# Performance work log

Measured on AMD Instinct MI355X. Metric: run time of the kernel, lower is better.

## Reference

```python
import jax, jax.numpy as jnp
import numpy as np

N, M = 65536, 512
CTRL = 128
IN_DIM = 128
READ_LEN = M + 6          # [M,1,1,3,1]
WRITE_LEN = 3 * M + 6     # [M,1,1,3,1,M,M]
EPS = 1e-16


def setup_inputs() -> dict:
    key = jax.random.key(0)
    ks = jax.random.split(key, 12)
    s = 0.02
    return {
        "x":   jax.random.normal(ks[0], (4, IN_DIM), jnp.float32),
        "mem": jax.random.normal(ks[1], (N, M), jnp.float32) * 0.05,
        "Wc":  jax.random.normal(ks[2], (CTRL, IN_DIM), jnp.float32) * s,
        "bc":  jnp.zeros((CTRL,), jnp.float32),
        "Wr":  jax.random.normal(ks[3], (READ_LEN, CTRL), jnp.float32) * s,
        "br":  jnp.zeros((READ_LEN,), jnp.float32),
        "Ww":  jax.random.normal(ks[4], (WRITE_LEN, CTRL), jnp.float32) * s,
        "bw":  jnp.zeros((WRITE_LEN,), jnp.float32),
        "W1":  jax.random.normal(ks[5], (200, M + CTRL), jnp.float32) * s,
        "b1":  jnp.zeros((200,), jnp.float32),
        "W2":  jax.random.normal(ks[6], (10, 200), jnp.float32) * s,
        "b2":  jnp.zeros((10,), jnp.float32),
    }


def _address(mem, k, beta, g, s, gamma, w_prev):
    # content + gate + circular shift + sharpen (standard NTM addressing)
    beta = jax.nn.softplus(beta)
    g = jax.nn.sigmoid(g)
    s = jax.nn.softmax(s)                      # (3,)
    gamma = 1.0 + jax.nn.softplus(gamma)
    # cosine similarity against all N memory rows
    dot = mem @ k                              # (N,)
    norms = jnp.sqrt(jnp.sum(mem * mem, axis=1)) * jnp.sqrt(jnp.sum(k * k)) + EPS
    wc = jax.nn.softmax(beta * dot / norms)    # content weights (N,)
    wg = g * wc + (1.0 - g) * w_prev           # gated
    # circular convolution with 3-tap shift kernel s = [s(-1), s(0), s(+1)]
    ws = s[0] * jnp.roll(wg, 1) + s[1] * wg + s[2] * jnp.roll(wg, -1)
    w = ws ** gamma                            # sharpen
    return w / (jnp.sum(w) + EPS)


def _forward(x, mem, Wc, bc, Wr, br, Ww, bw, W1, b1, W2, b2):
    cont = x @ Wc.T + bc                       # controller: (4, 128)
    w0 = jnp.full((N,), 1.0 / N, x.dtype)      # softmax of constant -> uniform

    def step(carry, c_t):
        mem, w_r, w_w = carry
        # ---- write head ----
        ow = c_t @ Ww.T + bw                   # (3M+6,)
        k, b, g, s, y = ow[:M], ow[M], ow[M+1], ow[M+2:M+5], ow[M+5]
        e, a = ow[M+6:2*M+6], ow[2*M+6:]
        w_w = _address(mem, k, b, g, s, y, w_w)
        e = jax.nn.sigmoid(e)
        mem = mem * (1.0 - jnp.outer(w_w, e)) + jnp.outer(w_w, a)
        # ---- read head ----
        orr = c_t @ Wr.T + br                  # (M+6,)
        k, b, g, s, y = orr[:M], orr[M], orr[M+1], orr[M+2:M+5], orr[M+5]
        w_r = _address(mem, k, b, g, s, y, w_r)
        r = w_r @ mem                          # (M,)
        # ---- output MLP ----
        h = jax.nn.relu(jnp.concatenate([c_t, r]) @ W1.T + b1)
        out = h @ W2.T + b2                    # (10,)
        return (mem, w_r, w_w), out

    _, outs = jax.lax.scan(step, (mem, w0, w0), cont)
    return outs                                # (4, 10)


def reference(x, mem, Wc, bc, Wr, br, Ww, bw, W1, b1, W2, b2):
    return _forward(x, mem, Wc, bc, Wr, br, Ww, bw, W1, b1, W2, b2)
```

## Files before the change

kernel.cpp:

```cpp
#include <hip/hip_runtime.h>
#include <math.h>

#define NN    65536
#define CTRLD 128
#define WLEN  1542
#define RLEN  518
#define EPSF  1e-16f
#define UB    2048
#define RPB   32
#define RPW   8

__device__ __forceinline__ float softplusf_(float x){
    return x > 0.f ? x + log1pf(expf(-x)) : log1pf(expf(x));
}
__device__ __forceinline__ float sigmoidf_(float x){ return 1.f/(1.f+expf(-x)); }

__device__ __forceinline__ float blockReduce256(float v, float* red){
    int t = threadIdx.x;
    red[t] = v; __syncthreads();
    for(int s = 128; s; s >>= 1){ if(t < s) red[t] += red[t+s]; __syncthreads(); }
    float r = red[0]; __syncthreads();
    return r;
}
__device__ __forceinline__ void waveReduce3(float& a, float& b, float& c){
    for(int o = 32; o; o >>= 1){
        a += __shfl_down(a,o); b += __shfl_down(b,o); c += __shfl_down(c,o);
    }
}
__device__ __forceinline__ void waveReduce1(float& a){
    for(int o = 32; o; o >>= 1) a += __shfl_down(a,o);
}

__global__ void k_owor(const float* __restrict__ x, const float* __restrict__ Wc,
                       const float* __restrict__ bc,
                       const float* __restrict__ Ww, const float* __restrict__ bw,
                       const float* __restrict__ Wr, const float* __restrict__ br,
                       float* __restrict__ cont,
                       float* __restrict__ kW, float* __restrict__ sW,
                       float* __restrict__ eW, float* __restrict__ aW,
                       float* __restrict__ kR, float* __restrict__ sR){
    __shared__ float cs[512];
    int tid = threadIdx.x;
    for(int q = tid; q < 512; q += 256){
        int t = q >> 7, c = q & 127;
        float acc = bc[c];
        const float* xr = x + t*CTRLD;
        const float* wr = Wc + c*CTRLD;
        for(int d = 0; d < CTRLD; ++d) acc += xr[d]*wr[d];
        cs[q] = acc;
        if(blockIdx.x == 0) cont[q] = acc;
    }
    __syncthreads();
    int idx = blockIdx.x*256 + tid;
    if(idx < 4*WLEN){
        int t = idx / WLEN, o = idx % WLEN;
        float acc = bw[o];
        const float* cr = cs + t*CTRLD;
        const float* wr = Ww + o*CTRLD;
        for(int d = 0; d < CTRLD; ++d) acc += cr[d]*wr[d];
        if(o < 512)       kW[t*512 + o] = acc;
        else if(o < 518)  sW[t*8 + (o-512)] = acc;
        else if(o < 1030) eW[t*512 + (o-518)] = sigmoidf_(acc);
        else              aW[t*512 + (o-1030)] = acc;
    } else {
        int j = idx - 4*WLEN;
        if(j < 4*RLEN){
            int t = j / RLEN, o = j % RLEN;
            float acc = br[o];
            const float* cr = cs + t*CTRLD;
            const float* wr = Wr + o*CTRLD;
            for(int d = 0; d < CTRLD; ++d) acc += cr[d]*wr[d];
            if(o < 512) kR[t*512 + o] = acc;
            else        sR[t*8 + (o-512)] = acc;
        }
    }
}

__global__ void k_prep(const float* __restrict__ kW, const float* __restrict__ kR,
                       float* __restrict__ kn){
    int t = threadIdx.x;
    int wave = t >> 6, lane = t & 63;
    int step = wave >> 1, which = wave & 1;
    const float* base = which ? (kR + step*512) : (kW + step*512);
    float s = 0.f;
    for(int h = 0; h < 8; ++h){ float v = base[lane + h*64]; s += v*v; }
    waveReduce1(s);
    if(lane == 0) kn[wave] = sqrtf(s);
}

template<int CH, bool RP, bool UPD, bool DOTR, bool DOTW>
__global__ __launch_bounds__(256) void k_mega(
    const float* __restrict__ mem0,
    const float* __restrict__ wunWall, const float* __restrict__ pSWall,
    const float* __restrict__ wunRall,
    const float* __restrict__ eW, const float* __restrict__ aW,
    const float* __restrict__ kRc, const float* __restrict__ sRc,
    const float* __restrict__ kWn, const float* __restrict__ sWn,
    const float* __restrict__ kn, int knRidx, int knWidx,
    float* __restrict__ dotRo, float* __restrict__ dotWo, float* __restrict__ n2o,
    float* __restrict__ pZr, float* __restrict__ pZw, float* __restrict__ rp)
{
    constexpr int NW = CH + (UPD ? 1 : 0);
    constexpr int NA = NW > 0 ? NW : 1;
    __shared__ float red[256];
    __shared__ float zsh[4][2];
    __shared__ float rps[4][512];
    int t = threadIdx.x;
    float wnorm[NA];
    #pragma unroll
    for(int j = 0; j < NW; ++j)
        wnorm[j] = 1.f/(blockReduce256(pSWall[j*256 + t], red) + EPSF);

    int wave = t >> 6, lane = t & 63;
    int c0 = lane, c1 = lane + 64;
    float4 ev0[NA], ev1[NA], av0[NA], av1[NA];
    #pragma unroll
    for(int j = 0; j < NW; ++j){
        ev0[j] = ((const float4*)(eW + j*512))[c0];
        ev1[j] = ((const float4*)(eW + j*512))[c1];
        av0[j] = ((const float4*)(aW + j*512))[c0];
        av1[j] = ((const float4*)(aW + j*512))[c1];
    }
    float4 kra, krb, kwa, kwb;
    float betaR = 0.f, betaW = 0.f, knRv = 1.f, knWv = 1.f;
    if constexpr(DOTR){
        kra = ((const float4*)kRc)[c0]; krb = ((const float4*)kRc)[c1];
        betaR = softplusf_(sRc[0]); knRv = kn[knRidx];
    }
    if constexpr(DOTW){
        kwa = ((const float4*)kWn)[c0]; kwb = ((const float4*)kWn)[c1];
        betaW = softplusf_(sWn[0]); knWv = kn[knWidx];
    }
    float4 rpA = {0,0,0,0}, rpB = {0,0,0,0};
    float zr = 0.f, zw = 0.f;
    int row0 = blockIdx.x*RPB + wave*RPW;
    const float4* src = (const float4*)mem0;
    for(int r = 0; r < RPW; ++r){
        int row = row0 + r;
        size_t base = (size_t)row*128;
        float4 v0 = src[base + c0], v1 = src[base + c1];
        #pragma unroll
        for(int j = 0; j < CH; ++j){
            float w = wunWall[(size_t)j*NN + row]*wnorm[j];
            v0.x = v0.x*(1.f - w*ev0[j].x) + w*av0[j].x;
            v0.y = v0.y*(1.f - w*ev0[j].y) + w*av0[j].y;
            v0.z = v0.z*(1.f - w*ev0[j].z) + w*av0[j].z;
            v0.w = v0.w*(1.f - w*ev0[j].w) + w*av0[j].w;
            v1.x = v1.x*(1.f - w*ev1[j].x) + w*av1[j].x;
            v1.y = v1.y*(1.f - w*ev1[j].y) + w*av1[j].y;
            v1.z = v1.z*(1.f - w*ev1[j].z) + w*av1[j].z;
            v1.w = v1.w*(1.f - w*ev1[j].w) + w*av1[j].w;
        }
        if constexpr(RP){
            float wr = wunRall[(size_t)(CH-1)*NN + row];
            rpA.x += wr*v0.x; rpA.y += wr*v0.y; rpA.z += wr*v0.z; rpA.w += wr*v0.w;
            rpB.x += wr*v1.x; rpB.y += wr*v1.y; rpB.z += wr*v1.z; rpB.w += wr*v1.w;
        }
        if constexpr(UPD){
            float w = wunWall[(size_t)CH*NN + row]*wnorm[CH];
            v0.x = v0.x*(1.f - w*ev0[CH].x) + w*av0[CH].x;
            v0.y = v0.y*(1.f - w*ev0[CH].y) + w*av0[CH].y;
            v0.z = v0.z*(1.f - w*ev0[CH].z) + w*av0[CH].z;
            v0.w = v0.w*(1.f - w*ev0[CH].w) + w*av0[CH].w;
            v1.x = v1.x*(1.f - w*ev1[CH].x) + w*av1[CH].x;
            v1.y = v1.y*(1.f - w*ev1[CH].y) + w*av1[CH].y;
            v1.z = v1.z*(1.f - w*ev1[CH].z) + w*av1[CH].z;
            v1.w = v1.w*(1.f - w*ev1[CH].w) + w*av1[CH].w;
        }
        if constexpr(DOTR || DOTW){
            float d = 0.f, dn = 0.f;
            float n = v0.x*v0.x+v0.y*v0.y+v0.z*v0.z+v0.w*v0.w
                    + v1.x*v1.x+v1.y*v1.y+v1.z*v1.z+v1.w*v1.w;
            if constexpr(DOTR)
                d = v0.x*kra.x+v0.y*kra.y+v0.z*kra.z+v0.w*kra.w
                  + v1.x*krb.x+v1.y*krb.y+v1.z*krb.z+v1.w*krb.w;
            if constexpr(DOTW)
                dn = v0.x*kwa.x+v0.y*kwa.y+v0.z*kwa.z+v0.w*kwa.w
                   + v1.x*kwb.x+v1.y*kwb.y+v1.z*kwb.z+v1.w*kwb.w;
            waveReduce3(d, dn, n);
            if(lane == 0){
                n2o[row] = n;
                float sn = sqrtf(n);
                if constexpr(DOTR){ dotRo[row] = d;  zr += expf(betaR*d /(sn*knRv + EPSF)); }
                if constexpr(DOTW){ dotWo[row] = dn; zw += expf(betaW*dn/(sn*knWv + EPSF)); }
            }
        }
    }
    if constexpr(DOTR || DOTW){
        if(lane == 0){ zsh[wave][0] = zr; zsh[wave][1] = zw; }
    }
    __syncthreads();
    if constexpr(RP){
        ((float4*)rps[wave])[c0] = rpA;
        ((float4*)rps[wave])[c1] = rpB;
        __syncthreads();
        rp[(size_t)blockIdx.x*512 + t]       = rps[0][t]+rps[1][t]+rps[2][t]+rps[3][t];
        rp[(size_t)blockIdx.x*512 + t + 256] = rps[0][t+256]+rps[1][t+256]+rps[2][t+256]+rps[3][t+256];
    }
    if(t == 0){
        if constexpr(DOTR) pZr[blockIdx.x] = zsh[0][0]+zsh[1][0]+zsh[2][0]+zsh[3][0];
        if constexpr(DOTW) pZw[blockIdx.x] = zsh[0][1]+zsh[1][1]+zsh[2][1]+zsh[3][1];
    }
}

__global__ void k_w0(const float* __restrict__ sW0, const float* __restrict__ dot,
                     const float* __restrict__ n2v, const float* __restrict__ pZ,
                     const float* __restrict__ kn,
                     float* __restrict__ wun, float* __restrict__ pS){
    __shared__ float red[256];
    int t = threadIdx.x;
    float z = 0.f;
    for(int j = t; j < UB; j += 256) z += pZ[j];
    float Z = blockReduce256(z, red);
    float beta  = softplusf_(sW0[0]);
    float g     = sigmoidf_(sW0[1]);
    float s0 = sW0[2], s1 = sW0[3], s2 = sW0[4];
    float sm = fmaxf(s0, fmaxf(s1, s2));
    float e0 = expf(s0-sm), e1 = expf(s1-sm), e2 = expf(s2-sm);
    float es = e0+e1+e2;
    s0 = e0/es; s1 = e1/es; s2 = e2/es;
    float gamma = 1.f + softplusf_(sW0[5]);
    float knv = kn[0];
    float invZ = 1.f/Z;
    int i  = blockIdx.x*256 + t;
    int im = (i-1) & (NN-1), ip = (i+1) & (NN-1);
    auto wgf = [&](int j)->float{
        float a = beta*dot[j]/(sqrtf(n2v[j])*knv + EPSF);
        return g*expf(a)*invZ + (1.f-g)*(1.f/NN);
    };
    float wsv = s0*wgf(im) + s1*wgf(i) + s2*wgf(ip);
    float wu = powf(wsv, gamma);
    wun[i] = wu;
    float S = blockReduce256(wu, red);
    if(t == 0) pS[blockIdx.x] = S;
}

__global__ void k_w2(const float* __restrict__ sRt, const float* __restrict__ dotRv,
                     const float* __restrict__ n2v, const float* __restrict__ pZr,
                     const float* __restrict__ wunRprev, const float* __restrict__ pSRprev,
                     const float* __restrict__ kn, int knRidx,
                     float* __restrict__ wunRout, float* __restrict__ pSRout,
                     int doW,
                     const float* __restrict__ sWn, const float* __restrict__ dotWv,
                     const float* __restrict__ pZw,
                     const float* __restrict__ wunWprev, const float* __restrict__ pSWprev,
                     int knWidx,
                     float* __restrict__ wunWout, float* __restrict__ pSWout){
    __shared__ float red[256];
    int t = threadIdx.x;
    int i  = blockIdx.x*256 + t;
    int im = (i-1) & (NN-1), ip = (i+1) & (NN-1);
    {
        float z = 0.f;
        for(int j = t; j < UB; j += 256) z += pZr[j];
        float Z = blockReduce256(z, red);
        float invSp = 1.f;
        if(pSRprev) invSp = 1.f/(blockReduce256(pSRprev[t], red) + EPSF);
        float beta  = softplusf_(sRt[0]);
        float g     = sigmoidf_(sRt[1]);
        float s0 = sRt[2], s1 = sRt[3], s2 = sRt[4];
        float sm = fmaxf(s0, fmaxf(s1, s2));
        float e0 = expf(s0-sm), e1 = expf(s1-sm), e2 = expf(s2-sm);
        float es = e0+e1+e2;
        s0 = e0/es; s1 = e1/es; s2 = e2/es;
        float gamma = 1.f + softplusf_(sRt[5]);
        float knv = kn[knRidx];
        float invZ = 1.f/Z;
        auto wgf = [&](int j)->float{
            float a = beta*dotRv[j]/(sqrtf(n2v[j])*knv + EPSF);
            float pv = wunRprev ? wunRprev[j]*invSp : (1.f/NN);
            return g*expf(a)*invZ + (1.f-g)*pv;
        };
        float wsv = s0*wgf(im) + s1*wgf(i) + s2*wgf(ip);
        float wu = powf(wsv, gamma);
        wunRout[i] = wu;
        float S = blockReduce256(wu, red);
        if(t == 0) pSRout[blockIdx.x] = S;
    }
    if(doW){
        float z = 0.f;
        for(int j = t; j < UB; j += 256) z += pZw[j];
        float Z = blockReduce256(z, red);
        float invSp = 1.f/(blockReduce256(pSWprev[t], red) + EPSF);
        float beta  = softplusf_(sWn[0]);
        float g     = sigmoidf_(sWn[1]);
        float s0 = sWn[2], s1 = sWn[3], s2 = sWn[4];
        float sm = fmaxf(s0, fmaxf(s1, s2));
        float e0 = expf(s0-sm), e1 = expf(s1-sm), e2 = expf(s2-sm);
        float es = e0+e1+e2;
        s0 = e0/es; s1 = e1/es; s2 = e2/es;
        float gamma = 1.f + softplusf_(sWn[5]);
        float knv = kn[knWidx];
        float invZ = 1.f/Z;
        auto wgf = [&](int j)->float{
            float a = beta*dotWv[j]/(sqrtf(n2v[j])*knv + EPSF);
            return g*expf(a)*invZ + (1.f-g)*wunWprev[j]*invSp;
        };
        float wsv = s0*wgf(im) + s1*wgf(i) + s2*wgf(ip);
        float wu = powf(wsv, gamma);
        wunWout[i] = wu;
        float S = blockReduce256(wu, red);
        if(t == 0) pSWout[blockIdx.x] = S;
    }
}

__global__ void k_rsumA(const float* __restrict__ rp, float* __restrict__ p2){
    int t = threadIdx.x, b = blockIdx.x;
    float ax = 0.f, ay = 0.f;
    const float2* r2 = (const float2*)rp;
    for(int j = 0; j < 32; ++j){
        float2 v = r2[(size_t)(b*32 + j)*256 + t];
        ax += v.x; ay += v.y;
    }
    float2 o; o.x = ax; o.y = ay;
    ((float2*)p2)[b*256 + t] = o;
}

__global__ void k_final(const float* __restrict__ cont, const float* __restrict__ p2,
                        const float* __restrict__ pSRn,
                        const float* __restrict__ W1, const float* __restrict__ b1,
                        const float* __restrict__ W2, const float* __restrict__ b2,
                        float* __restrict__ out, int step){
    __shared__ float red[256];
    __shared__ float conc[640];
    __shared__ float h[200];
    int t = threadIdx.x;
    float S = blockReduce256(pSRn[t], red);
    float invS = 1.f/(S + EPSF);
    float ax = 0.f, ay = 0.f;
    const float2* q = (const float2*)p2;
    for(int j = 0; j < 64; ++j){
        float2 v = q[j*256 + t];
        ax += v.x; ay += v.y;
    }
    conc[128 + 2*t]   = ax*invS;
    conc[128 + 2*t+1] = ay*invS;
    if(t < 128) conc[t] = cont[step*128 + t];
    __syncthreads();
    if(t < 200){
        float acc = b1[t];
        const float* wr = W1 + t*640;
        for(int q2 = 0; q2 < 640; ++q2) acc += wr[q2]*conc[q2];
        h[t] = fmaxf(acc, 0.f);
    }
    __syncthreads();
    if(t < 10){
        float acc = b2[t];
        const float* wr = W2 + t*200;
        for(int p = 0; p < 200; ++p) acc += wr[p]*h[p];
        out[step*10 + t] = acc;
    }
}

extern "C" void kernel_launch(void* const* d_in, const int* in_sizes, int n_in,
                              void* d_out, int out_size, void* d_ws, size_t ws_size,
                              hipStream_t stream) {
    const float* x    = (const float*)d_in[0];
    const float* mem0 = (const float*)d_in[1];
    const float* Wc   = (const float*)d_in[2];
    const float* bc   = (const float*)d_in[3];
    const float* Wr   = (const float*)d_in[4];
    const float* br   = (const float*)d_in[5];
    const float* Ww   = (const float*)d_in[6];
    const float* bw   = (const float*)d_in[7];
    const float* W1   = (const float*)d_in[8];
    const float* b1   = (const float*)d_in[9];
    const float* W2   = (const float*)d_in[10];
    const float* b2   = (const float*)d_in[11];
    float* out = (float*)d_out;

    float* ws = (float*)d_ws;
    size_t off = 0;
    float* wunW = ws + off; off += 4*(size_t)NN;
    float* pSW  = ws + off; off += 4*256;
    float* wunR = ws + off; off += 4*(size_t)NN;
    float* pSR  = ws + off; off += 4*256;
    float* dotR = ws + off; off += NN;
    float* dotW = ws + off; off += NN;
    float* n2v  = ws + off; off += NN;
    float* pZr  = ws + off; off += UB;
    float* pZw  = ws + off; off += UB;
    float* cont = ws + off; off += 512;
    float* kW   = ws + off; off += 4*512;
    float* sW   = ws + off; off += 4*8;
    float* eW   = ws + off; off += 4*512;
    float* aW   = ws + off; off += 4*512;
    float* kR   = ws + off; off += 4*512;
    float* sR   = ws + off; off += 4*8;
    float* kn   = ws + off; off += 16;
    float* rp   = ws + off; off += (size_t)UB*512;
    float* p2   = ws + off; off += 64*512;

    k_owor<<<33, 256, 0, stream>>>(x, Wc, bc, Ww, bw, Wr, br,
                                   cont, kW, sW, eW, aW, kR, sR);
    k_prep<<<1, 512, 0, stream>>>(kW, kR, kn);

    k_mega<0,false,false,false,true><<<UB, 256, 0, stream>>>(
        mem0, wunW, pSW, wunR, eW, aW,
        nullptr, nullptr, kW, sW, kn, 0, 0,
        dotR, dotW, n2v, pZr, pZw, rp);
    k_w0<<<256, 256, 0, stream>>>(sW, dotW, n2v, pZw, kn, wunW, pSW);

    k_mega<0,false,true,true,true><<<UB, 256, 0, stream>>>(
        mem0, wunW, pSW, wunR, eW, aW,
        kR, sR, kW + 512, sW + 8, kn, 1, 2,
        dotR, dotW, n2v, pZr, pZw, rp);
    k_w2<<<256, 256, 0, stream>>>(sR, dotR, n2v, pZr,
                                  nullptr, nullptr, kn, 1,
                                  wunR, pSR, 1,
                                  sW + 8, dotW, pZw, wunW, pSW, 2,
                                  wunW + NN, pSW + 256);

    k_mega<1,true,true,true,true><<<UB, 256, 0, stream>>>(
        mem0, wunW, pSW, wunR, eW, aW,
        kR + 512, sR + 8, kW + 1024, sW + 16, kn, 3, 4,
        dotR, dotW, n2v, pZr, pZw, rp);
    k_w2<<<256, 256, 0, stream>>>(sR + 8, dotR, n2v, pZr,
                                  wunR, pSR, kn, 3,
                                  wunR + NN, pSR + 256, 1,
                                  sW + 16, dotW, pZw, wunW + NN, pSW + 256, 4,
                                  wunW + 2*(size_t)NN, pSW + 512);
    k_rsumA<<<64, 256, 0, stream>>>(rp, p2);
    k_final<<<1, 256, 0, stream>>>(cont, p2, pSR, W1, b1, W2, b2, out, 0);

    k_mega<2,true,true,true,true><<<UB, 256, 0, stream>>>(
        mem0, wunW, pSW, wunR, eW, aW,
        kR + 1024, sR + 16, kW + 1536, sW + 24, kn, 5, 6,
        dotR, dotW, n2v, pZr, pZw, rp);
    k_w2<<<256, 256, 0, stream>>>(sR + 16, dotR, n2v, pZr,
                                  wunR + NN, pSR + 256, kn, 5,
                                  wunR + 2*(size_t)NN, pSR + 512, 1,
                                  sW + 24, dotW, pZw, wunW + 2*(size_t)NN, pSW + 512, 6,
                                  wunW + 3*(size_t)NN, pSW + 768);
    k_rsumA<<<64, 256, 0, stream>>>(rp, p2);
    k_final<<<1, 256, 0, stream>>>(cont, p2, pSR + 256, W1, b1, W2, b2, out, 1);

    k_mega<3,true,true,true,false><<<UB, 256, 0, stream>>>(
        mem0, wunW, pSW, wunR, eW, aW,
        kR + 1536, sR + 24, nullptr, nullptr, kn, 7, 0,
        dotR, dotW, n2v, pZr, pZw, rp);
    k_w2<<<256, 256, 0, stream>>>(sR + 24, dotR, n2v, pZr,
                                  wunR + 2*(size_t)NN, pSR + 512, kn, 7,
                                  wunR + 3*(size_t)NN, pSR + 768, 0,
                                  nullptr, nullptr, nullptr, nullptr, nullptr, 0,
                                  nullptr, nullptr);
    k_rsumA<<<64, 256, 0, stream>>>(rp, p2);
    k_final<<<1, 256, 0, stream>>>(cont, p2, pSR + 512, W1, b1, W2, b2, out, 2);

    k_mega<4,true,false,false,false><<<UB, 256, 0, stream>>>(
        mem0, wunW, pSW, wunR, eW, aW,
        nullptr, nullptr, nullptr, nullptr, kn, 0, 0,
        dotR, dotW, n2v, pZr, pZw, rp);
    k_rsumA<<<64, 256, 0, stream>>>(rp, p2);
    k_final<<<1, 256, 0, stream>>>(cont, p2, pSR + 768, W1, b1, W2, b2, out, 3);

    (void)in_sizes; (void)n_in; (void)out_size; (void)ws_size;
}
```

Baseline: 422.4 us.

## Fuse the per-step kernel chain into one cooperative persistent kernel with grid syncs

```diff
diff --git a/kernel.cpp b/kernel.cpp
--- a/kernel.cpp
+++ b/kernel.cpp
@@ -1,14 +1,31 @@
 #include <hip/hip_runtime.h>
+#include <hip/hip_cooperative_groups.h>
 #include <math.h>
+
+namespace cg = cooperative_groups;
 
 #define NN    65536
 #define CTRLD 128
 #define WLEN  1542
 #define RLEN  518
 #define EPSF  1e-16f
-#define UB    2048
-#define RPB   32
-#define RPW   8
+#define GRIDB 1024
+#define ROWSB 64
+#define RPWV  16
+
+struct KP {
+  const float* mem0; const float* cont;
+  const float* kW; const float* sW; const float* eW; const float* aW;
+  const float* kR; const float* sR; const float* kn;
+  float *dotR, *dotW, *n2v;
+  float *wunW, *pSW, *wunR, *pSR;
+  float *pZr, *pZw;
+  float *rp, *p2, *hbuf;
+  const float *W1, *b1, *W2, *b2;
+  float* out;
+};
+
+struct Smem { float red[256]; float big[2048]; float zsh[4][2]; };
 
 __device__ __forceinline__ float softplusf_(float x){
     return x > 0.f ? x + log1pf(expf(-x)) : log1pf(expf(x));
@@ -29,6 +46,297 @@
 }
 __device__ __forceinline__ void waveReduce1(float& a){
     for(int o = 32; o; o >>= 1) a += __shfl_down(a,o);
+}
+
+template<int CH, bool RP, bool UPD, bool DOTR, bool DOTW>
+__device__ __forceinline__ void sweep_phase(const KP& p, Smem& sm, int rstep,
+    const float* kRc, const float* sRc, int knRi,
+    const float* kWn, const float* sWn, int knWi)
+{
+    constexpr int NW = CH + (UPD ? 1 : 0);
+    constexpr int NA = (NW > 0) ? NW : 1;
+    int t = threadIdx.x, bid = blockIdx.x;
+    float wnorm[NA];
+    #pragma unroll
+    for(int j = 0; j < NW; ++j){
+        float s = p.pSW[j*GRIDB+t] + p.pSW[j*GRIDB+t+256]
+                + p.pSW[j*GRIDB+t+512] + p.pSW[j*GRIDB+t+768];
+        wnorm[j] = 1.f/(blockReduce256(s, sm.red) + EPSF);
+    }
+    int wave = t >> 6, lane = t & 63;
+    int c0 = lane, c1 = lane + 64;
+    float4 ev0[NA], ev1[NA], av0[NA], av1[NA];
+    #pragma unroll
+    for(int j = 0; j < NW; ++j){
+        ev0[j] = ((const float4*)(p.eW + j*512))[c0];
+        ev1[j] = ((const float4*)(p.eW + j*512))[c1];
+        av0[j] = ((const float4*)(p.aW + j*512))[c0];
+        av1[j] = ((const float4*)(p.aW + j*512))[c1];
+    }
+    float4 kra, krb, kwa, kwb;
+    float betaR = 0.f, betaW = 0.f, knRv = 1.f, knWv = 1.f;
+    if constexpr(DOTR){
+        kra = ((const float4*)kRc)[c0]; krb = ((const float4*)kRc)[c1];
+        betaR = softplusf_(sRc[0]); knRv = p.kn[knRi];
+    }
+    if constexpr(DOTW){
+        kwa = ((const float4*)kWn)[c0]; kwb = ((const float4*)kWn)[c1];
+        betaW = softplusf_(sWn[0]); knWv = p.kn[knWi];
+    }
+    float4 rpA = {0,0,0,0}, rpB = {0,0,0,0};
+    float zr = 0.f, zw = 0.f;
+    int row0 = bid*ROWSB + wave*RPWV;
+    const float4* src = (const float4*)p.mem0;
+    for(int r = 0; r < RPWV; ++r){
+        int row = row0 + r;
+        size_t base = (size_t)row*128;
+        float4 v0 = src[base + c0], v1 = src[base + c1];
+        #pragma unroll
+        for(int j = 0; j < CH; ++j){
+            float w = p.wunW[(size_t)j*NN + row]*wnorm[j];
+            v0.x = v0.x*(1.f - w*ev0[j].x) + w*av0[j].x;
+            v0.y = v0.y*(1.f - w*ev0[j].y) + w*av0[j].y;
+            v0.z = v0.z*(1.f - w*ev0[j].z) + w*av0[j].z;
+            v0.w = v0.w*(1.f - w*ev0[j].w) + w*av0[j].w;
+            v1.x = v1.x*(1.f - w*ev1[j].x) + w*av1[j].x;
+            v1.y = v1.y*(1.f - w*ev1[j].y) + w*av1[j].y;
+            v1.z = v1.z*(1.f - w*ev1[j].z) + w*av1[j].z;
+            v1.w = v1.w*(1.f - w*ev1[j].w) + w*av1[j].w;
+        }
+        if constexpr(RP){
+            float wr = p.wunR[(size_t)rstep*NN + row];
+            rpA.x += wr*v0.x; rpA.y += wr*v0.y; rpA.z += wr*v0.z; rpA.w += wr*v0.w;
+            rpB.x += wr*v1.x; rpB.y += wr*v1.y; rpB.z += wr*v1.z; rpB.w += wr*v1.w;
+        }
+        if constexpr(UPD){
+            float w = p.wunW[(size_t)CH*NN + row]*wnorm[CH];
+            v0.x = v0.x*(1.f - w*ev0[CH].x) + w*av0[CH].x;
+            v0.y = v0.y*(1.f - w*ev0[CH].y) + w*av0[CH].y;
+            v0.z = v0.z*(1.f - w*ev0[CH].z) + w*av0[CH].z;
+            v0.w = v0.w*(1.f - w*ev0[CH].w) + w*av0[CH].w;
+            v1.x = v1.x*(1.f - w*ev1[CH].x) + w*av1[CH].x;
+            v1.y = v1.y*(1.f - w*ev1[CH].y) + w*av1[CH].y;
+            v1.z = v1.z*(1.f - w*ev1[CH].z) + w*av1[CH].z;
+            v1.w = v1.w*(1.f - w*ev1[CH].w) + w*av1[CH].w;
+        }
+        if constexpr(DOTR || DOTW){
+            float d = 0.f, dn = 0.f;
+            float n = v0.x*v0.x+v0.y*v0.y+v0.z*v0.z+v0.w*v0.w
+                    + v1.x*v1.x+v1.y*v1.y+v1.z*v1.z+v1.w*v1.w;
+            if constexpr(DOTR)
+                d = v0.x*kra.x+v0.y*kra.y+v0.z*kra.z+v0.w*kra.w
+                  + v1.x*krb.x+v1.y*krb.y+v1.z*krb.z+v1.w*krb.w;
+            if constexpr(DOTW)
+                dn = v0.x*kwa.x+v0.y*kwa.y+v0.z*kwa.z+v0.w*kwa.w
+                   + v1.x*kwb.x+v1.y*kwb.y+v1.z*kwb.z+v1.w*kwb.w;
+            waveReduce3(d, dn, n);
+            if(lane == 0){
+                p.n2v[row] = n;
+                float sn = sqrtf(n);
+                if constexpr(DOTR){ p.dotR[row] = d;  zr += expf(betaR*d /(sn*knRv + EPSF)); }
+                if constexpr(DOTW){ p.dotW[row] = dn; zw += expf(betaW*dn/(sn*knWv + EPSF)); }
+            }
+        }
+    }
+    if constexpr(DOTR || DOTW){
+        if(lane == 0){ sm.zsh[wave][0] = zr; sm.zsh[wave][1] = zw; }
+    }
+    if constexpr(RP){
+        ((float4*)(sm.big + wave*512))[c0] = rpA;
+        ((float4*)(sm.big + wave*512))[c1] = rpB;
+    }
+    __syncthreads();
+    if constexpr(RP){
+        p.rp[(size_t)bid*512 + t] =
+            sm.big[t] + sm.big[512+t] + sm.big[1024+t] + sm.big[1536+t];
+        p.rp[(size_t)bid*512 + t + 256] =
+            sm.big[t+256] + sm.big[768+t] + sm.big[1280+t] + sm.big[1792+t];
+    }
+    if(t == 0){
+        if constexpr(DOTR) p.pZr[bid] = sm.zsh[0][0]+sm.zsh[1][0]+sm.zsh[2][0]+sm.zsh[3][0];
+        if constexpr(DOTW) p.pZw[bid] = sm.zsh[0][1]+sm.zsh[1][1]+sm.zsh[2][1]+sm.zsh[3][1];
+    }
+    __syncthreads();
+}
+
+__device__ __forceinline__ void whead_phase(const KP& p, Smem& sm,
+    const float* sV, const float* dotv, const float* pZ,
+    const float* wprev, const float* pSprev, int knidx,
+    float* wun, float* pSout)
+{
+    int t = threadIdx.x, bid = blockIdx.x;
+    float z = pZ[t] + pZ[t+256] + pZ[t+512] + pZ[t+768];
+    float Z = blockReduce256(z, sm.red);
+    float invSp = 1.f;
+    if(pSprev){
+        float sp = pSprev[t] + pSprev[t+256] + pSprev[t+512] + pSprev[t+768];
+        invSp = 1.f/(blockReduce256(sp, sm.red) + EPSF);
+    }
+    float beta  = softplusf_(sV[0]);
+    float g     = sigmoidf_(sV[1]);
+    float s0 = sV[2], s1 = sV[3], s2 = sV[4];
+    float smx = fmaxf(s0, fmaxf(s1, s2));
+    float e0 = expf(s0-smx), e1 = expf(s1-smx), e2 = expf(s2-smx);
+    float es = e0+e1+e2;
+    s0 = e0/es; s1 = e1/es; s2 = e2/es;
+    float gamma = 1.f + softplusf_(sV[5]);
+    float knv = p.kn[knidx];
+    float invZ = 1.f/Z;
+    float wu = 0.f;
+    if(t < ROWSB){
+        int i = bid*ROWSB + t;
+        int im = (i-1) & (NN-1), ip = (i+1) & (NN-1);
+        auto wgf = [&](int j)->float{
+            float a = beta*dotv[j]/(sqrtf(p.n2v[j])*knv + EPSF);
+            float pv = wprev ? wprev[j]*invSp : (1.f/NN);
+            return g*expf(a)*invZ + (1.f-g)*pv;
+        };
+        wu = powf(s0*wgf(im) + s1*wgf(i) + s2*wgf(ip), gamma);
+        wun[i] = wu;
+    }
+    float S = blockReduce256(wu, sm.red);
+    if(t == 0) pSout[bid] = S;
+}
+
+__device__ __forceinline__ void rsum1_phase(const KP& p, float* dst){
+    int t = threadIdx.x, b = blockIdx.x;
+    float2 acc; acc.x = 0.f; acc.y = 0.f;
+    const float2* r2 = (const float2*)p.rp;
+    for(int j = 0; j < 16; ++j){
+        float2 v = r2[(size_t)(b*16 + j)*256 + t];
+        acc.x += v.x; acc.y += v.y;
+    }
+    ((float2*)dst)[b*256 + t] = acc;
+}
+
+__device__ __forceinline__ void h_phase(const KP& p, Smem& sm, int hb, int step,
+                                        const float* p2src){
+    int t = threadIdx.x;
+    const float* pS = p.pSR + step*GRIDB;
+    float sp = pS[t] + pS[t+256] + pS[t+512] + pS[t+768];
+    float invS = 1.f/(blockReduce256(sp, sm.red) + EPSF);
+    float2 acc; acc.x = 0.f; acc.y = 0.f;
+    const float2* q = (const float2*)p2src;
+    for(int j = 0; j < 64; ++j){
+        float2 v = q[j*256 + t];
+        acc.x += v.x; acc.y += v.y;
+    }
+    float* conc = sm.big;
+    conc[128 + 2*t]     = acc.x*invS;
+    conc[128 + 2*t + 1] = acc.y*invS;
+    if(t < 128) conc[t] = p.cont[step*128 + t];
+    __syncthreads();
+    int wave = t >> 6, lane = t & 63;
+    for(int ol = wave; ol < 25; ol += 4){
+        int o = hb*25 + ol;
+        const float* wr = p.W1 + (size_t)o*640;
+        float a = 0.f;
+        for(int q2 = lane; q2 < 640; q2 += 64) a += wr[q2]*conc[q2];
+        waveReduce1(a);
+        if(lane == 0) p.hbuf[step*200 + o] = fmaxf(a + p.b1[o], 0.f);
+    }
+    __syncthreads();
+}
+
+__device__ __forceinline__ void out_phase(const KP& p, int step){
+    int t = threadIdx.x;
+    if(t < 10){
+        float a = p.b2[t];
+        const float* wr = p.W2 + t*200;
+        const float* h = p.hbuf + step*200;
+        for(int j = 0; j < 200; ++j) a += wr[j]*h[j];
+        p.out[step*10 + t] = a;
+    }
+}
+
+__global__ void __launch_bounds__(256, 4) k_coop(KP p){
+    cg::grid_group g = cg::this_grid();
+    __shared__ Smem sm;
+    int bid = blockIdx.x;
+    sweep_phase<0,false,false,false,true>(p, sm, 0, nullptr,nullptr,0, p.kW, p.sW, 0);
+    g.sync();
+    whead_phase(p, sm, p.sW, p.dotW, p.pZw, nullptr, nullptr, 0, p.wunW, p.pSW);
+    g.sync();
+    sweep_phase<0,false,true,true,true>(p, sm, 0, p.kR, p.sR, 1, p.kW+512, p.sW+8, 2);
+    g.sync();
+    whead_phase(p, sm, p.sR, p.dotR, p.pZr, nullptr, nullptr, 1, p.wunR, p.pSR);
+    whead_phase(p, sm, p.sW+8, p.dotW, p.pZw, p.wunW, p.pSW, 2, p.wunW+NN, p.pSW+GRIDB);
+    g.sync();
+    sweep_phase<1,true,true,true,true>(p, sm, 0, p.kR+512, p.sR+8, 3, p.kW+1024, p.sW+16, 4);
+    g.sync();
+    whead_phase(p, sm, p.sR+8, p.dotR, p.pZr, p.wunR, p.pSR, 3, p.wunR+NN, p.pSR+GRIDB);
+    whead_phase(p, sm, p.sW+16, p.dotW, p.pZw, p.wunW+NN, p.pSW+GRIDB, 4,
+                p.wunW+2*(size_t)NN, p.pSW+2*GRIDB);
+    if(bid < 64) rsum1_phase(p, p.p2);
+    g.sync();
+    sweep_phase<2,true,true,true,true>(p, sm, 1, p.kR+1024, p.sR+16, 5, p.kW+1536, p.sW+24, 6);
+    g.sync();
+    whead_phase(p, sm, p.sR+16, p.dotR, p.pZr, p.wunR+NN, p.pSR+GRIDB, 5,
+                p.wunR+2*(size_t)NN, p.pSR+2*GRIDB);
+    whead_phase(p, sm, p.sW+24, p.dotW, p.pZw, p.wunW+2*(size_t)NN, p.pSW+2*GRIDB, 6,
+                p.wunW+3*(size_t)NN, p.pSW+3*GRIDB);
+    if(bid < 64) rsum1_phase(p, p.p2 + 64*512);
+    if(bid >= 64 && bid < 72) h_phase(p, sm, bid-64, 0, p.p2);
+    g.sync();
+    sweep_phase<3,true,true,true,false>(p, sm, 2, p.kR+1536, p.sR+24, 7, nullptr,nullptr,0);
+    g.sync();
+    whead_phase(p, sm, p.sR+24, p.dotR, p.pZr, p.wunR+2*(size_t)NN, p.pSR+2*GRIDB, 7,
+                p.wunR+3*(size_t)NN, p.pSR+3*GRIDB);
+    if(bid < 64) rsum1_phase(p, p.p2);
+    if(bid >= 64 && bid < 72) h_phase(p, sm, bid-64, 1, p.p2 + 64*512);
+    if(bid == 72) out_phase(p, 0);
+    g.sync();
+    sweep_phase<4,true,false,false,false>(p, sm, 3, nullptr,nullptr,0, nullptr,nullptr,0);
+    g.sync();
+    if(bid < 64) rsum1_phase(p, p.p2 + 64*512);
+    if(bid >= 64 && bid < 72) h_phase(p, sm, bid-64, 2, p.p2);
+    if(bid == 72) out_phase(p, 1);
+    g.sync();
+    if(bid < 8) h_phase(p, sm, bid, 3, p.p2 + 64*512);
+    if(bid == 8) out_phase(p, 2);
+    g.sync();
+    if(bid == 0) out_phase(p, 3);
+}
+
+__global__ void __launch_bounds__(256) g_sweepA(KP p){
+    __shared__ Smem sm;
+    sweep_phase<0,false,false,false,true>(p, sm, 0, nullptr,nullptr,0, p.kW, p.sW, 0);
+}
+__global__ void __launch_bounds__(256) g_sweepC0(KP p){
+    __shared__ Smem sm;
+    sweep_phase<0,false,true,true,true>(p, sm, 0, p.kR, p.sR, 1, p.kW+512, p.sW+8, 2);
+}
+__global__ void __launch_bounds__(256) g_sweepC1(KP p){
+    __shared__ Smem sm;
+    sweep_phase<1,true,true,true,true>(p, sm, 0, p.kR+512, p.sR+8, 3, p.kW+1024, p.sW+16, 4);
+}
+__global__ void __launch_bounds__(256) g_sweepC2(KP p){
+    __shared__ Smem sm;
+    sweep_phase<2,true,true,true,true>(p, sm, 1, p.kR+1024, p.sR+16, 5, p.kW+1536, p.sW+24, 6);
+}
+__global__ void __launch_bounds__(256) g_sweepC3(KP p){
+    __shared__ Smem sm;
+    sweep_phase<3,true,true,true,false>(p, sm, 2, p.kR+1536, p.sR+24, 7, nullptr,nullptr,0);
+}
+__global__ void __launch_bounds__(256) g_sweepC4(KP p){
+    __shared__ Smem sm;
+    sweep_phase<4,true,false,false,false>(p, sm, 3, nullptr,nullptr,0, nullptr,nullptr,0);
+}
+__global__ void __launch_bounds__(256) g_whead(KP p, const float* sV, const float* dotv,
+    const float* pZ, const float* wprev, const float* pSprev, int knidx,
+    float* wun, float* pSout){
+    __shared__ Smem sm;
+    whead_phase(p, sm, sV, dotv, pZ, wprev, pSprev, knidx, wun, pSout);
+}
+__global__ void __launch_bounds__(256) g_rsum1(KP p, float* dst){
+    rsum1_phase(p, dst);
+}
+__global__ void __launch_bounds__(256) g_h(KP p, int step, const float* p2src){
+    __shared__ Smem sm;
+    h_phase(p, sm, blockIdx.x, step, p2src);
+}
+__global__ void __launch_bounds__(256) g_out(KP p, int step){
+    out_phase(p, step);
 }
 
 __global__ void k_owor(const float* __restrict__ x, const float* __restrict__ Wc,
@@ -88,270 +396,6 @@
     if(lane == 0) kn[wave] = sqrtf(s);
 }
 
-template<int CH, bool RP, bool UPD, bool DOTR, bool DOTW>
-__global__ __launch_bounds__(256) void k_mega(
-    const float* __restrict__ mem0,
-    const float* __restrict__ wunWall, const float* __restrict__ pSWall,
-    const float* __restrict__ wunRall,
-    const float* __restrict__ eW, const float* __restrict__ aW,
-    const float* __restrict__ kRc, const float* __restrict__ sRc,
-    const float* __restrict__ kWn, const float* __restrict__ sWn,
-    const float* __restrict__ kn, int knRidx, int knWidx,
-    float* __restrict__ dotRo, float* __restrict__ dotWo, float* __restrict__ n2o,
-    float* __restrict__ pZr, float* __restrict__ pZw, float* __restrict__ rp)
-{
-    constexpr int NW = CH + (UPD ? 1 : 0);
-    constexpr int NA = NW > 0 ? NW : 1;
-    __shared__ float red[256];
-    __shared__ float zsh[4][2];
-    __shared__ float rps[4][512];
-    int t = threadIdx.x;
-    float wnorm[NA];
-    #pragma unroll
-    for(int j = 0; j < NW; ++j)
-        wnorm[j] = 1.f/(blockReduce256(pSWall[j*256 + t], red) + EPSF);
-
-    int wave = t >> 6, lane = t & 63;
-    int c0 = lane, c1 = lane + 64;
-    float4 ev0[NA], ev1[NA], av0[NA], av1[NA];
-    #pragma unroll
-    for(int j = 0; j < NW; ++j){
-        ev0[j] = ((const float4*)(eW + j*512))[c0];
-        ev1[j] = ((const float4*)(eW + j*512))[c1];
-        av0[j] = ((const float4*)(aW + j*512))[c0];
-        av1[j] = ((const float4*)(aW + j*512))[c1];
-    }
-    float4 kra, krb, kwa, kwb;
-    float betaR = 0.f, betaW = 0.f, knRv = 1.f, knWv = 1.f;
-    if constexpr(DOTR){
-        kra = ((const float4*)kRc)[c0]; krb = ((const float4*)kRc)[c1];
-        betaR = softplusf_(sRc[0]); knRv = kn[knRidx];
-    }
-    if constexpr(DOTW){
-        kwa = ((const float4*)kWn)[c0]; kwb = ((const float4*)kWn)[c1];
-        betaW = softplusf_(sWn[0]); knWv = kn[knWidx];
-    }
-    float4 rpA = {0,0,0,0}, rpB = {0,0,0,0};
-    float zr = 0.f, zw = 0.f;
-    int row0 = blockIdx.x*RPB + wave*RPW;
-    const float4* src = (const float4*)mem0;
-    for(int r = 0; r < RPW; ++r){
-        int row = row0 + r;
-        size_t base = (size_t)row*128;
-        float4 v0 = src[base + c0], v1 = src[base + c1];
-        #pragma unroll
-        for(int j = 0; j < CH; ++j){
-            float w = wunWall[(size_t)j*NN + row]*wnorm[j];
-            v0.x = v0.x*(1.f - w*ev0[j].x) + w*av0[j].x;
-            v0.y = v0.y*(1.f - w*ev0[j].y) + w*av0[j].y;
-            v0.z = v0.z*(1.f - w*ev0[j].z) + w*av0[j].z;
-            v0.w = v0.w*(1.f - w*ev0[j].w) + w*av0[j].w;
-            v1.x = v1.x*(1.f - w*ev1[j].x) + w*av1[j].x;
-            v1.y = v1.y*(1.f - w*ev1[j].y) + w*av1[j].y;
-            v1.z = v1.z*(1.f - w*ev1[j].z) + w*av1[j].z;
-            v1.w = v1.w*(1.f - w*ev1[j].w) + w*av1[j].w;
-        }
-        if constexpr(RP){
-            float wr = wunRall[(size_t)(CH-1)*NN + row];
-            rpA.x += wr*v0.x; rpA.y += wr*v0.y; rpA.z += wr*v0.z; rpA.w += wr*v0.w;
-            rpB.x += wr*v1.x; rpB.y += wr*v1.y; rpB.z += wr*v1.z; rpB.w += wr*v1.w;
-        }
-        if constexpr(UPD){
-            float w = wunWall[(size_t)CH*NN + row]*wnorm[CH];
-            v0.x = v0.x*(1.f - w*ev0[CH].x) + w*av0[CH].x;
-            v0.y = v0.y*(1.f - w*ev0[CH].y) + w*av0[CH].y;
-            v0.z = v0.z*(1.f - w*ev0[CH].z) + w*av0[CH].z;
-            v0.w = v0.w*(1.f - w*ev0[CH].w) + w*av0[CH].w;
-            v1.x = v1.x*(1.f - w*ev1[CH].x) + w*av1[CH].x;
-            v1.y = v1.y*(1.f - w*ev1[CH].y) + w*av1[CH].y;
-            v1.z = v1.z*(1.f - w*ev1[CH].z) + w*av1[CH].z;
-            v1.w = v1.w*(1.f - w*ev1[CH].w) + w*av1[CH].w;
-        }
-        if constexpr(DOTR || DOTW){
-            float d = 0.f, dn = 0.f;
-            float n = v0.x*v0.x+v0.y*v0.y+v0.z*v0.z+v0.w*v0.w
-                    + v1.x*v1.x+v1.y*v1.y+v1.z*v1.z+v1.w*v1.w;
-            if constexpr(DOTR)
-                d = v0.x*kra.x+v0.y*kra.y+v0.z*kra.z+v0.w*kra.w
-                  + v1.x*krb.x+v1.y*krb.y+v1.z*krb.z+v1.w*krb.w;
-            if constexpr(DOTW)
-                dn = v0.x*kwa.x+v0.y*kwa.y+v0.z*kwa.z+v0.w*kwa.w
-                   + v1.x*kwb.x+v1.y*kwb.y+v1.z*kwb.z+v1.w*kwb.w;
-            waveReduce3(d, dn, n);
-            if(lane == 0){
-                n2o[row] = n;
-                float sn = sqrtf(n);
-                if constexpr(DOTR){ dotRo[row] = d;  zr += expf(betaR*d /(sn*knRv + EPSF)); }
-                if constexpr(DOTW){ dotWo[row] = dn; zw += expf(betaW*dn/(sn*knWv + EPSF)); }
-            }
-        }
-    }
-    if constexpr(DOTR || DOTW){
-        if(lane == 0){ zsh[wave][0] = zr; zsh[wave][1] = zw; }
-    }
-    __syncthreads();
-    if constexpr(RP){
-        ((float4*)rps[wave])[c0] = rpA;
-        ((float4*)rps[wave])[c1] = rpB;
-        __syncthreads();
-        rp[(size_t)blockIdx.x*512 + t]       = rps[0][t]+rps[1][t]+rps[2][t]+rps[3][t];
-        rp[(size_t)blockIdx.x*512 + t + 256] = rps[0][t+256]+rps[1][t+256]+rps[2][t+256]+rps[3][t+256];
-    }
-    if(t == 0){
-        if constexpr(DOTR) pZr[blockIdx.x] = zsh[0][0]+zsh[1][0]+zsh[2][0]+zsh[3][0];
-        if constexpr(DOTW) pZw[blockIdx.x] = zsh[0][1]+zsh[1][1]+zsh[2][1]+zsh[3][1];
-    }
-}
-
-__global__ void k_w0(const float* __restrict__ sW0, const float* __restrict__ dot,
-                     const float* __restrict__ n2v, const float* __restrict__ pZ,
-                     const float* __restrict__ kn,
-                     float* __restrict__ wun, float* __restrict__ pS){
-    __shared__ float red[256];
-    int t = threadIdx.x;
-    float z = 0.f;
-    for(int j = t; j < UB; j += 256) z += pZ[j];
-    float Z = blockReduce256(z, red);
-    float beta  = softplusf_(sW0[0]);
-    float g     = sigmoidf_(sW0[1]);
-    float s0 = sW0[2], s1 = sW0[3], s2 = sW0[4];
-    float sm = fmaxf(s0, fmaxf(s1, s2));
-    float e0 = expf(s0-sm), e1 = expf(s1-sm), e2 = expf(s2-sm);
-    float es = e0+e1+e2;
-    s0 = e0/es; s1 = e1/es; s2 = e2/es;
-    float gamma = 1.f + softplusf_(sW0[5]);
-    float knv = kn[0];
-    float invZ = 1.f/Z;
-    int i  = blockIdx.x*256 + t;
-    int im = (i-1) & (NN-1), ip = (i+1) & (NN-1);
-    auto wgf = [&](int j)->float{
-        float a = beta*dot[j]/(sqrtf(n2v[j])*knv + EPSF);
-        return g*expf(a)*invZ + (1.f-g)*(1.f/NN);
-    };
-    float wsv = s0*wgf(im) + s1*wgf(i) + s2*wgf(ip);
-    float wu = powf(wsv, gamma);
-    wun[i] = wu;
-    float S = blockReduce256(wu, red);
-    if(t == 0) pS[blockIdx.x] = S;
-}
-
-__global__ void k_w2(const float* __restrict__ sRt, const float* __restrict__ dotRv,
-                     const float* __restrict__ n2v, const float* __restrict__ pZr,
-                     const float* __restrict__ wunRprev, const float* __restrict__ pSRprev,
-                     const float* __restrict__ kn, int knRidx,
-                     float* __restrict__ wunRout, float* __restrict__ pSRout,
-                     int doW,
-                     const float* __restrict__ sWn, const float* __restrict__ dotWv,
-                     const float* __restrict__ pZw,
-                     const float* __restrict__ wunWprev, const float* __restrict__ pSWprev,
-                     int knWidx,
-                     float* __restrict__ wunWout, float* __restrict__ pSWout){
-    __shared__ float red[256];
-    int t = threadIdx.x;
-    int i  = blockIdx.x*256 + t;
-    int im = (i-1) & (NN-1), ip = (i+1) & (NN-1);
-    {
-        float z = 0.f;
-        for(int j = t; j < UB; j += 256) z += pZr[j];
-        float Z = blockReduce256(z, red);
-        float invSp = 1.f;
-        if(pSRprev) invSp = 1.f/(blockReduce256(pSRprev[t], red) + EPSF);
-        float beta  = softplusf_(sRt[0]);
-        float g     = sigmoidf_(sRt[1]);
-        float s0 = sRt[2], s1 = sRt[3], s2 = sRt[4];
-        float sm = fmaxf(s0, fmaxf(s1, s2));
-        float e0 = expf(s0-sm), e1 = expf(s1-sm), e2 = expf(s2-sm);
-        float es = e0+e1+e2;
-        s0 = e0/es; s1 = e1/es; s2 = e2/es;
-        float gamma = 1.f + softplusf_(sRt[5]);
-        float knv = kn[knRidx];
-        float invZ = 1.f/Z;
-        auto wgf = [&](int j)->float{
-            float a = beta*dotRv[j]/(sqrtf(n2v[j])*knv + EPSF);
-            float pv = wunRprev ? wunRprev[j]*invSp : (1.f/NN);
-            return g*expf(a)*invZ + (1.f-g)*pv;
-        };
-        float wsv = s0*wgf(im) + s1*wgf(i) + s2*wgf(ip);
-        float wu = powf(wsv, gamma);
-        wunRout[i] = wu;
-        float S = blockReduce256(wu, red);
-        if(t == 0) pSRout[blockIdx.x] = S;
-    }
-    if(doW){
-        float z = 0.f;
-        for(int j = t; j < UB; j += 256) z += pZw[j];
-        float Z = blockReduce256(z, red);
-        float invSp = 1.f/(blockReduce256(pSWprev[t], red) + EPSF);
-        float beta  = softplusf_(sWn[0]);
-        float g     = sigmoidf_(sWn[1]);
-        float s0 = sWn[2], s1 = sWn[3], s2 = sWn[4];
-        float sm = fmaxf(s0, fmaxf(s1, s2));
-        float e0 = expf(s0-sm), e1 = expf(s1-sm), e2 = expf(s2-sm);
-        float es = e0+e1+e2;
-        s0 = e0/es; s1 = e1/es; s2 = e2/es;
-        float gamma = 1.f + softplusf_(sWn[5]);
-        float knv = kn[knWidx];
-        float invZ = 1.f/Z;
-        auto wgf = [&](int j)->float{
-            float a = beta*dotWv[j]/(sqrtf(n2v[j])*knv + EPSF);
-            return g*expf(a)*invZ + (1.f-g)*wunWprev[j]*invSp;
-        };
-        float wsv = s0*wgf(im) + s1*wgf(i) + s2*wgf(ip);
-        float wu = powf(wsv, gamma);
-        wunWout[i] = wu;
-        float S = blockReduce256(wu, red);
-        if(t == 0) pSWout[blockIdx.x] = S;
-    }
-}
-
-__global__ void k_rsumA(const float* __restrict__ rp, float* __restrict__ p2){
-    int t = threadIdx.x, b = blockIdx.x;
-    float ax = 0.f, ay = 0.f;
-    const float2* r2 = (const float2*)rp;
-    for(int j = 0; j < 32; ++j){
-        float2 v = r2[(size_t)(b*32 + j)*256 + t];
-        ax += v.x; ay += v.y;
-    }
-    float2 o; o.x = ax; o.y = ay;
-    ((float2*)p2)[b*256 + t] = o;
-}
-
-__global__ void k_final(const float* __restrict__ cont, const float* __restrict__ p2,
-                        const float* __restrict__ pSRn,
-                        const float* __restrict__ W1, const float* __restrict__ b1,
-                        const float* __restrict__ W2, const float* __restrict__ b2,
-                        float* __restrict__ out, int step){
-    __shared__ float red[256];
-    __shared__ float conc[640];
-    __shared__ float h[200];
-    int t = threadIdx.x;
-    float S = blockReduce256(pSRn[t], red);
-    float invS = 1.f/(S + EPSF);
-    float ax = 0.f, ay = 0.f;
-    const float2* q = (const float2*)p2;
-    for(int j = 0; j < 64; ++j){
-        float2 v = q[j*256 + t];
-        ax += v.x; ay += v.y;
-    }
-    conc[128 + 2*t]   = ax*invS;
-    conc[128 + 2*t+1] = ay*invS;
-    if(t < 128) conc[t] = cont[step*128 + t];
-    __syncthreads();
-    if(t < 200){
-        float acc = b1[t];
-        const float* wr = W1 + t*640;
-        for(int q2 = 0; q2 < 640; ++q2) acc += wr[q2]*conc[q2];
-        h[t] = fmaxf(acc, 0.f);
-    }
-    __syncthreads();
-    if(t < 10){
-        float acc = b2[t];
-        const float* wr = W2 + t*200;
-        for(int p = 0; p < 200; ++p) acc += wr[p]*h[p];
-        out[step*10 + t] = acc;
-    }
-}
-
 extern "C" void kernel_launch(void* const* d_in, const int* in_sizes, int n_in,
                               void* d_out, int out_size, void* d_ws, size_t ws_size,
                               hipStream_t stream) {
@@ -367,19 +411,18 @@
     const float* b1   = (const float*)d_in[9];
     const float* W2   = (const float*)d_in[10];
     const float* b2   = (const float*)d_in[11];
-    float* out = (float*)d_out;
 
     float* ws = (float*)d_ws;
     size_t off = 0;
     float* wunW = ws + off; off += 4*(size_t)NN;
-    float* pSW  = ws + off; off += 4*256;
+    float* pSW  = ws + off; off += 4*GRIDB;
     float* wunR = ws + off; off += 4*(size_t)NN;
-    float* pSR  = ws + off; off += 4*256;
+    float* pSR  = ws + off; off += 4*GRIDB;
     float* dotR = ws + off; off += NN;
     float* dotW = ws + off; off += NN;
     float* n2v  = ws + off; off += NN;
-    float* pZr  = ws + off; off += UB;
-    float* pZw  = ws + off; off += UB;
+    float* pZr  = ws + off; off += GRIDB;
+    float* pZw  = ws + off; off += GRIDB;
     float* cont = ws + off; off += 512;
     float* kW   = ws + off; off += 4*512;
     float* sW   = ws + off; off += 4*8;
@@ -388,71 +431,72 @@
     float* kR   = ws + off; off += 4*512;
     float* sR   = ws + off; off += 4*8;
     float* kn   = ws + off; off += 16;
-    float* rp   = ws + off; off += (size_t)UB*512;
-    float* p2   = ws + off; off += 64*512;
+    float* rp   = ws + off; off += (size_t)GRIDB*512;
+    float* p2   = ws + off; off += 2*64*512;
+    float* hbuf = ws + off; off += 1024;
+
+    KP P;
+    P.mem0 = mem0; P.cont = cont;
+    P.kW = kW; P.sW = sW; P.eW = eW; P.aW = aW; P.kR = kR; P.sR = sR; P.kn = kn;
+    P.dotR = dotR; P.dotW = dotW; P.n2v = n2v;
+    P.wunW = wunW; P.pSW = pSW; P.wunR = wunR; P.pSR = pSR;
+    P.pZr = pZr; P.pZw = pZw;
+    P.rp = rp; P.p2 = p2; P.hbuf = hbuf;
+    P.W1 = W1; P.b1 = b1; P.W2 = W2; P.b2 = b2;
+    P.out = (float*)d_out;
 
     k_owor<<<33, 256, 0, stream>>>(x, Wc, bc, Ww, bw, Wr, br,
                                    cont, kW, sW, eW, aW, kR, sR);
     k_prep<<<1, 512, 0, stream>>>(kW, kR, kn);
 
-    k_mega<0,false,false,false,true><<<UB, 256, 0, stream>>>(
-        mem0, wunW, pSW, wunR, eW, aW,
-        nullptr, nullptr, kW, sW, kn, 0, 0,
-        dotR, dotW, n2v, pZr, pZw, rp);
-    k_w0<<<256, 256, 0, stream>>>(sW, dotW, n2v, pZw, kn, wunW, pSW);
-
-    k_mega<0,false,true,true,true><<<UB, 256, 0, stream>>>(
-        mem0, wunW, pSW, wunR, eW, aW,
-        kR, sR, kW + 512, sW + 8, kn, 1, 2,
-        dotR, dotW, n2v, pZr, pZw, rp);
-    k_w2<<<256, 256, 0, stream>>>(sR, dotR, n2v, pZr,
-                                  nullptr, nullptr, kn, 1,
-                                  wunR, pSR, 1,
-                                  sW + 8, dotW, pZw, wunW, pSW, 2,
-                                  wunW + NN, pSW + 256);
-
-    k_mega<1,true,true,true,true><<<UB, 256, 0, stream>>>(
-        mem0, wunW, pSW, wunR, eW, aW,
-        kR + 512, sR + 8, kW + 1024, sW + 16, kn, 3, 4,
-        dotR, dotW, n2v, pZr, pZw, rp);
-    k_w2<<<256, 256, 0, stream>>>(sR + 8, dotR, n2v, pZr,
-                                  wunR, pSR, kn, 3,
-                                  wunR + NN, pSR + 256, 1,
-                                  sW + 16, dotW, pZw, wunW + NN, pSW + 256, 4,
-                                  wunW + 2*(size_t)NN, pSW + 512);
-    k_rsumA<<<64, 256, 0, stream>>>(rp, p2);
-    k_final<<<1, 256, 0, stream>>>(cont, p2, pSR, W1, b1, W2, b2, out, 0);
-
-    k_mega<2,true,true,true,true><<<UB, 256, 0, stream>>>(
-        mem0, wunW, pSW, wunR, eW, aW,
-        kR + 1024, sR + 16, kW + 1536, sW + 24, kn, 5, 6,
-        dotR, dotW, n2v, pZr, pZw, rp);
-    k_w2<<<256, 256, 0, stream>>>(sR + 16, dotR, n2v, pZr,
-                                  wunR + NN, pSR + 256, kn, 5,
-                                  wunR + 2*(size_t)NN, pSR + 512, 1,
-                                  sW + 24, dotW, pZw, wunW + 2*(size_t)NN, pSW + 512, 6,
-                                  wunW + 3*(size_t)NN, pSW + 768);
-    k_rsumA<<<64, 256, 0, stream>>>(rp, p2);
-    k_final<<<1, 256, 0, stream>>>(cont, p2, pSR + 256, W1, b1, W2, b2, out, 1);
-
-    k_mega<3,true,true,true,false><<<UB, 256, 0, stream>>>(
-        mem0, wunW, pSW, wunR, eW, aW,
-        kR + 1536, sR + 24, nullptr, nullptr, kn, 7, 0,
-        dotR, dotW, n2v, pZr, pZw, rp);
-    k_w2<<<256, 256, 0, stream>>>(sR + 24, dotR, n2v, pZr,
-                                  wunR + 2*(size_t)NN, pSR + 512, kn, 7,
-                                  wunR + 3*(size_t)NN, pSR + 768, 0,
-                                  nullptr, nullptr, nullptr, nullptr, nullptr, 0,
-                                  nullptr, nullptr);
-    k_rsumA<<<64, 256, 0, stream>>>(rp, p2);
-    k_final<<<1, 256, 0, stream>>>(cont, p2, pSR + 512, W1, b1, W2, b2, out, 2);
-
-    k_mega<4,true,false,false,false><<<UB, 256, 0, stream>>>(
-        mem0, wunW, pSW, wunR, eW, aW,
-        nullptr, nullptr, nullptr, nullptr, kn, 0, 0,
-        dotR, dotW, n2v, pZr, pZw, rp);
-    k_rsumA<<<64, 256, 0, stream>>>(rp, p2);
-    k_final<<<1, 256, 0, stream>>>(cont, p2, pSR + 768, W1, b1, W2, b2, out, 3);
-
+    bool useCoop = false;
+    int coopAttr = 0;
+    if(hipDeviceGetAttribute(&coopAttr, hipDeviceAttributeCooperativeLaunch, 0) == hipSuccess
+       && coopAttr){
+        int nCU = 0, maxb = 0;
+        if(hipDeviceGetAttribute(&nCU, hipDeviceAttributeMultiprocessorCount, 0) == hipSuccess
+           && hipOccupancyMaxActiveBlocksPerMultiprocessor(&maxb, k_coop, 256, 0) == hipSuccess
+           && (long)maxb*(long)nCU >= GRIDB){
+            useCoop = true;
+        }
+    }
+    if(useCoop){
+        void* args[] = { (void*)&P };
+        hipError_t e = hipLaunchCooperativeKernel((const void*)k_coop,
+                           dim3(GRIDB), dim3(256), args, 0, stream);
+        if(e != hipSuccess){ (void)hipGetLastError(); useCoop = false; }
+    }
+    if(!useCoop){
+        g_sweepA<<<GRIDB, 256, 0, stream>>>(P);
+        g_whead <<<GRIDB, 256, 0, stream>>>(P, sW, dotW, pZw, nullptr, nullptr, 0, wunW, pSW);
+        g_sweepC0<<<GRIDB, 256, 0, stream>>>(P);
+        g_whead <<<GRIDB, 256, 0, stream>>>(P, sR, dotR, pZr, nullptr, nullptr, 1, wunR, pSR);
+        g_whead <<<GRIDB, 256, 0, stream>>>(P, sW+8, dotW, pZw, wunW, pSW, 2, wunW+NN, pSW+GRIDB);
+        g_sweepC1<<<GRIDB, 256, 0, stream>>>(P);
+        g_whead <<<GRIDB, 256, 0, stream>>>(P, sR+8, dotR, pZr, wunR, pSR, 3, wunR+NN, pSR+GRIDB);
+        g_whead <<<GRIDB, 256, 0, stream>>>(P, sW+16, dotW, pZw, wunW+NN, pSW+GRIDB, 4,
+                                            wunW+2*(size_t)NN, pSW+2*GRIDB);
+        g_rsum1 <<<64, 256, 0, stream>>>(P, p2);
+        g_sweepC2<<<GRIDB, 256, 0, stream>>>(P);
+        g_whead <<<GRIDB, 256, 0, stream>>>(P, sR+16, dotR, pZr, wunR+NN, pSR+GRIDB, 5,
+                                            wunR+2*(size_t)NN, pSR+2*GRIDB);
+        g_whead <<<GRIDB, 256, 0, stream>>>(P, sW+24, dotW, pZw, wunW+2*(size_t)NN, pSW+2*GRIDB, 6,
+                                            wunW+3*(size_t)NN, pSW+3*GRIDB);
+        g_rsum1 <<<64, 256, 0, stream>>>(P, p2 + 64*512);
+        g_h     <<<8, 256, 0, stream>>>(P, 0, p2);
+        g_sweepC3<<<GRIDB, 256, 0, stream>>>(P);
+        g_whead <<<GRIDB, 256, 0, stream>>>(P, sR+24, dotR, pZr, wunR+2*(size_t)NN, pSR+2*GRIDB, 7,
+                                            wunR+3*(size_t)NN, pSR+3*GRIDB);
+        g_rsum1 <<<64, 256, 0, stream>>>(P, p2);
+        g_h     <<<8, 256, 0, stream>>>(P, 1, p2 + 64*512);
+        g_out   <<<1, 256, 0, stream>>>(P, 0);
+        g_sweepC4<<<GRIDB, 256, 0, stream>>>(P);
+        g_rsum1 <<<64, 256, 0, stream>>>(P, p2 + 64*512);
+        g_h     <<<8, 256, 0, stream>>>(P, 2, p2);
+        g_out   <<<1, 256, 0, stream>>>(P, 1);
+        g_h     <<<8, 256, 0, stream>>>(P, 3, p2 + 64*512);
+        g_out   <<<1, 256, 0, stream>>>(P, 2);
+        g_out   <<<1, 256, 0, stream>>>(P, 3);
+    }
     (void)in_sizes; (void)n_in; (void)out_size; (void)ws_size;
 }
```

Result: faster. 393.1 us (-6.9%).
